# Optimization experiments

Measured on AMD Instinct MI355X. Metric: run time of the kernel, lower is better.

Reference implementation:

```python
import jax, jax.numpy as jnp
from jax import lax
import numpy as np


def _cum_masks(nd):
    # 4 nested cumulative masks over a 9-tap kernel: borders p=3,2,1,0
    ms = []
    for p in (3, 2, 1, 0):
        m = np.zeros((9,) * nd, np.float32)
        sl = tuple(slice(p, 9 - p) for _ in range(nd))
        m[sl] = 1.0
        ms.append(m)
    return jnp.asarray(np.stack(ms))  # (4, 9) or (4, 9, 9)


def _group_norm(x, w, b, groups, eps=1e-5):
    B, C, H, W = x.shape
    xg = x.reshape(B, groups, C // groups, H, W)
    mu = jnp.mean(xg, axis=(2, 3, 4), keepdims=True)
    var = jnp.var(xg, axis=(2, 3, 4), keepdims=True)
    xg = (xg - mu) * lax.rsqrt(var + eps)
    return xg.reshape(B, C, H, W) * w[None, :, None, None] + b[None, :, None, None]


def setup_inputs() -> dict:
    key = jax.random.key(0)
    ks = jax.random.split(key, 16)
    C = 256
    c = C // 4
    x = jax.random.normal(ks[0], (16, C, 128, 128), jnp.float32)
    W1 = jax.random.normal(ks[1], (1, 1, 9, 1, 1), jnp.float32)
    W2 = jax.random.normal(ks[2], (c, 1, 9, 9), jnp.float32)
    conv1_w = jax.random.normal(ks[3], (c, C, 1, 1), jnp.float32) * 0.05
    conv1_b = jax.random.normal(ks[4], (c,), jnp.float32) * 0.05
    conv2_w = jax.random.normal(ks[5], (C, c, 1, 1), jnp.float32) * 0.05
    conv2_b = jax.random.normal(ks[6], (C,), jnp.float32) * 0.05
    gn1_w = jnp.ones((c,), jnp.float32)
    gn1_b = jnp.zeros((c,), jnp.float32)
    gns_w = jnp.ones((c,), jnp.float32)
    gns_b = jnp.zeros((c,), jnp.float32)
    gn2_w = jnp.ones((C,), jnp.float32)
    gn2_b = jnp.zeros((C,), jnp.float32)
    return dict(x=x, W1=W1, W2=W2, conv1_w=conv1_w, conv1_b=conv1_b,
                conv2_w=conv2_w, conv2_b=conv2_b, gn1_w=gn1_w, gn1_b=gn1_b,
                gns_w=gns_w, gns_b=gns_b, gn2_w=gn2_w, gn2_b=gn2_b)


def reference(x, W1, W2, conv1_w, conv1_b, conv2_w, conv2_b,
              gn1_w, gn1_b, gns_w, gns_b, gn2_w, gn2_b):
    res = x
    # 1x1 conv + GN (bottleneck)
    h1 = jnp.einsum('bchw,oc->bohw', x, conv1_w[:, :, 0, 0]) + conv1_b[None, :, None, None]
    h1 = _group_norm(h1, gn1_w, gn1_b, 16)
    c = h1.shape[1]

    # --- branch A: multi-ring 1D conv along channel dim (conv3d, kernel (9,1,1)) ---
    m1 = _cum_masks(1)                                   # (4,9) cumulative masks
    r1 = m1 - jnp.concatenate([jnp.zeros_like(m1[:1]), m1[:-1]], 0)  # rings
    k1 = W1[0, 0, :, 0, 0]                               # (9,)
    a1 = jax.nn.softmax(jnp.sum(k1[None, :] * r1, 1) / (jnp.sum(r1, 1) + 1e-10))
    # linearity: softmax-weighted sum of 4 masked convs == one conv with weighted mask
    W1_eff = W1 * jnp.sum(a1[:, None] * m1, 0)[None, None, :, None, None]
    x3 = lax.conv_general_dilated(
        h1[:, None], W1_eff, (1, 1, 1), [(4, 4), (0, 0), (0, 0)],
        dimension_numbers=('NCDHW', 'OIDHW', 'NCDHW'))[:, 0]  # (b,c,h,w)

    # --- branch B: multi-ring 9x9 depthwise conv2d ---
    m2 = _cum_masks(2)                                   # (4,9,9)
    r2 = m2 - jnp.concatenate([jnp.zeros_like(m2[:1]), m2[:-1]], 0)
    num2 = jnp.sum(W2[None] * r2[:, None, None], axis=(1, 2, 3, 4))
    den2 = c * jnp.sum(r2, axis=(1, 2)) + 1e-10          # mask is (c,1,9,9) in torch
    a2 = jax.nn.softmax(num2 / den2)
    W2_eff = W2 * jnp.sum(a2[:, None, None] * m2, 0)[None, None]
    x_sa = lax.conv_general_dilated(
        h1, W2_eff, (1, 1), [(4, 4), (4, 4)],
        dimension_numbers=('NCHW', 'OIHW', 'NCHW'), feature_group_count=c)

    h = jax.nn.relu(_group_norm(x3 + x_sa, gns_w, gns_b, 16))
    out = jnp.einsum('bchw,oc->bohw', h, conv2_w[:, :, 0, 0]) + conv2_b[None, :, None, None]
    out = jax.nn.relu(_group_norm(out, gn2_w, gn2_b, 16))
    return out + res
```

## Files before the change

kernel.cpp:

```cpp
#include <hip/hip_runtime.h>
#include <math.h>

#define HW   16384
#define CC   256
#define cC   64
#define BB   16
#define CHW  (CC*HW)
#define cHW  (cC*HW)

#define WS_TB    0
#define WS_H1B   8388608
#define WS_RAWB  16777216
#define WS_W2E   50331648
#define WS_K1E   (WS_W2E + 5184)
#define WS_GN1A  (WS_K1E + 16)
#define WS_GNSA  (WS_GN1A + 512)
#define WS_GN2A  (WS_GNSA + 512)
#define WS_W1P   (WS_GN2A + 512)
#define WS_W2P   (WS_W1P + 8192)

typedef __attribute__((ext_vector_type(8))) short bf16x8;
typedef __attribute__((ext_vector_type(4))) float f32x4;

__device__ inline unsigned short f2bf(float f) {
    union { float f; unsigned u; } c; c.f = f;
    unsigned r = c.u + 0x7FFFu + ((c.u >> 16) & 1u);
    return (unsigned short)(r >> 16);
}
__device__ inline float bf2f(unsigned short h) {
    union { unsigned u; float f; } c; c.u = ((unsigned)h) << 16; return c.f;
}

__global__ void k_setup(const float* __restrict__ W1, const float* __restrict__ W2,
                        const float* __restrict__ c1w, const float* __restrict__ c2w,
                        float* __restrict__ k1e, float* __restrict__ w2e,
                        float* __restrict__ accz, unsigned short* __restrict__ w1p,
                        unsigned short* __restrict__ w2p) {
    __shared__ float tapsum[81];
    __shared__ float a2s[4];
    int tdx = threadIdx.x;
    for (int i = tdx; i < 1536; i += 128) accz[i] = 0.f;
    for (int e = tdx; e < 16384; e += 128) {
        int fi = e >> 9, rem = e & 511;
        int l = rem >> 3, j = rem & 7;
        int ks = fi >> 2, nf = fi & 3;
        int c = ks * 32 + (l >> 4) * 8 + j;
        int oc = nf * 16 + (l & 15);
        w1p[e] = f2bf(c1w[oc * 256 + c]);
    }
    for (int e = tdx; e < 16384; e += 128) {
        int fi = e >> 9, rem = e & 511;
        int l = rem >> 3, j = rem & 7;
        int ks = fi >> 4, nfg = fi & 15;
        int c = ks * 32 + (l >> 4) * 8 + j;
        int oc = nfg * 16 + (l & 15);
        w2p[e] = f2bf(c2w[oc * 64 + c]);
    }
    if (tdx < 81) {
        float s = 0.f;
        for (int ch = 0; ch < 64; ++ch) s += W2[ch * 81 + tdx];
        tapsum[tdx] = s;
    }
    __syncthreads();
    if (tdx == 0) {
        float ring[4] = {0.f, 0.f, 0.f, 0.f};
        for (int i = 0; i < 9; ++i)
            for (int j = 0; j < 9; ++j) {
                int d = max(abs(i - 4), abs(j - 4));
                int r = (d <= 1) ? 0 : (d - 1);
                ring[r] += tapsum[i * 9 + j];
            }
        float den2[4] = {576.f, 1024.f, 1536.f, 2048.f};
        float v[4], mx = -1e30f;
        for (int p = 0; p < 4; ++p) { v[p] = ring[p] / den2[p]; mx = fmaxf(mx, v[p]); }
        float se = 0.f;
        for (int p = 0; p < 4; ++p) { v[p] = expf(v[p] - mx); se += v[p]; }
        for (int p = 0; p < 4; ++p) a2s[p] = v[p] / se;
        float k1[9];
        for (int k = 0; k < 9; ++k) k1[k] = W1[k];
        float num[4];
        num[0] = k1[3] + k1[4] + k1[5];
        num[1] = k1[2] + k1[6];
        num[2] = k1[1] + k1[7];
        num[3] = k1[0] + k1[8];
        float den1[4] = {3.f, 2.f, 2.f, 2.f};
        mx = -1e30f;
        for (int p = 0; p < 4; ++p) { v[p] = num[p] / den1[p]; mx = fmaxf(mx, v[p]); }
        se = 0.f;
        for (int p = 0; p < 4; ++p) { v[p] = expf(v[p] - mx); se += v[p]; }
        float a1[4];
        for (int p = 0; p < 4; ++p) a1[p] = v[p] / se;
        float s1arr[5];
        s1arr[0] = 1.f; s1arr[1] = 1.f;
        s1arr[4] = a1[3]; s1arr[3] = a1[2] + a1[3]; s1arr[2] = a1[1] + s1arr[3];
        for (int k = 0; k < 9; ++k) { int d = abs(k - 4); k1e[k] = k1[k] * s1arr[d]; }
    }
    __syncthreads();
    float s2arr[5];
    s2arr[0] = 1.f; s2arr[1] = 1.f;
    s2arr[4] = a2s[3]; s2arr[3] = a2s[2] + a2s[3]; s2arr[2] = a2s[1] + s2arr[3];
    for (int idx = tdx; idx < 64 * 81; idx += 128) {
        int tap = idx % 81;
        int i = tap / 9, j = tap - i * 9;
        int d = max(abs(i - 4), abs(j - 4));
        w2e[idx] = W2[idx] * s2arr[d];
    }
}

__device__ inline void gn_affine(const float* __restrict__ acc, int b, int g,
                                 float inv_n, const float* __restrict__ gw,
                                 const float* __restrict__ gb, int ch,
                                 float& sc, float& sh) {
    float s = acc[(b * 16 + g) * 2], ss = acc[(b * 16 + g) * 2 + 1];
    float mu = s * inv_n;
    float var = ss * inv_n - mu * mu;
    float rstd = rsqrtf(var + 1e-5f);
    sc = gw[ch] * rstd;
    sh = gb[ch] - mu * sc;
}

__global__ __launch_bounds__(256) void k_conv1(const float* __restrict__ x,
        const unsigned short* __restrict__ w1p, const float* __restrict__ b1,
        unsigned short* __restrict__ h1, float* __restrict__ gn1a) {
    int bid = blockIdx.x;
    int b = bid >> 6, pt = bid & 63;
    int tid = threadIdx.x;
    int w = tid >> 6, lane = tid & 63;
    int l15 = lane & 15, lg = lane >> 4;
    int p_wave = pt * 256 + w * 64;
    const bf16x8* w1v = (const bf16x8*)w1p;
    f32x4 acc[4][4];
#pragma unroll
    for (int mf = 0; mf < 4; ++mf)
#pragma unroll
        for (int nf = 0; nf < 4; ++nf) acc[mf][nf] = (f32x4){0.f, 0.f, 0.f, 0.f};
    const float* xb = x + b * CHW;
#pragma unroll 1
    for (int ks = 0; ks < 8; ++ks) {
        int c0 = ks * 32 + lg * 8;
        bf16x8 afr[4];
#pragma unroll
        for (int mf = 0; mf < 4; ++mf) {
            const float* xp = xb + c0 * HW + p_wave + mf * 16 + l15;
            bf16x8 a;
#pragma unroll
            for (int j = 0; j < 8; ++j) a[j] = (short)f2bf(__builtin_nontemporal_load(xp + j * HW));
            afr[mf] = a;
        }
#pragma unroll
        for (int nf = 0; nf < 4; ++nf) {
            bf16x8 bfr = w1v[(ks * 4 + nf) * 64 + lane];
#pragma unroll
            for (int mf = 0; mf < 4; ++mf)
                acc[mf][nf] = __builtin_amdgcn_mfma_f32_16x16x32_bf16(afr[mf], bfr, acc[mf][nf], 0, 0, 0);
        }
    }
    __shared__ float red[4][16][2];
    unsigned short* hb = h1 + b * cHW;
#pragma unroll
    for (int nf = 0; nf < 4; ++nf) {
        int oc = nf * 16 + l15;
        float bias = b1[oc];
        float s = 0.f, ss = 0.f;
#pragma unroll
        for (int mf = 0; mf < 4; ++mf) {
            f32x4 v = acc[mf][nf];
            v[0] += bias; v[1] += bias; v[2] += bias; v[3] += bias;
            ushort4 hv = make_ushort4(f2bf(v[0]), f2bf(v[1]), f2bf(v[2]), f2bf(v[3]));
            *(ushort4*)(hb + oc * HW + p_wave + mf * 16 + lg * 4) = hv;
            s += v[0] + v[1] + v[2] + v[3];
            ss += v[0] * v[0] + v[1] * v[1] + v[2] * v[2] + v[3] * v[3];
        }
        s += __shfl_xor(s, 16, 64); ss += __shfl_xor(ss, 16, 64);
        s += __shfl_xor(s, 32, 64); ss += __shfl_xor(ss, 32, 64);
        s += __shfl_xor(s, 1, 64);  ss += __shfl_xor(ss, 1, 64);
        s += __shfl_xor(s, 2, 64);  ss += __shfl_xor(ss, 2, 64);
        if (lg == 0 && (l15 & 3) == 0) {
            int g = nf * 4 + (l15 >> 2);
            red[w][g][0] = s; red[w][g][1] = ss;
        }
    }
    __syncthreads();
    if (tid < 32) {
        int g = tid >> 1, c = tid & 1;
        float v = red[0][g][c] + red[1][g][c] + red[2][g][c] + red[3][g][c];
        atomicAdd(&gn1a[(b * 16 + g) * 2 + c], v);
    }
}

__global__ __launch_bounds__(256) void k_x3(const unsigned short* __restrict__ h1,
        const float* __restrict__ gn1a, const float* __restrict__ g1w,
        const float* __restrict__ g1b, const float* __restrict__ k1e,
        unsigned short* __restrict__ t) {
    int i = blockIdx.x * 256 + threadIdx.x;
    int b = i >> 13, p = (i & 8191) * 2;
    __shared__ float lsc[64], lsh[64], lke[9];
    if (threadIdx.x < 64) {
        int ch = threadIdx.x;
        float sc, sh;
        gn_affine(gn1a, b, ch >> 2, 1.f / 65536.f, g1w, g1b, ch, sc, sh);
        lsc[ch] = sc; lsh[ch] = sh;
    }
    if (threadIdx.x < 9) lke[threadIdx.x] = k1e[threadIdx.x];
    __syncthreads();
    const unsigned short* hb = h1 + b * cHW + p;
    float2 win[9];
#pragma unroll
    for (int k = 0; k < 9; ++k) {
        int ch = k - 4;
        if (ch >= 0) {
            ushort2 hv = *(const ushort2*)(hb + ch * HW);
            float s = lsc[ch], h = lsh[ch];
            win[k] = make_float2(fmaf(bf2f(hv.x), s, h), fmaf(bf2f(hv.y), s, h));
        } else win[k] = make_float2(0.f, 0.f);
    }
    unsigned short* tb = t + b * cHW + p;
#pragma unroll
    for (int ch = 0; ch < 64; ++ch) {
        float2 s = make_float2(0.f, 0.f);
#pragma unroll
        for (int k = 0; k < 9; ++k) {
            float kv = lke[k];
            s.x = fmaf(win[k].x, kv, s.x);
            s.y = fmaf(win[k].y, kv, s.y);
        }
        *(ushort2*)(tb + ch * HW) = make_ushort2(f2bf(s.x), f2bf(s.y));
#pragma unroll
        for (int k = 0; k < 8; ++k) win[k] = win[k + 1];
        int nc = ch + 5;
        if (nc < 64) {
            ushort2 hv = *(const ushort2*)(hb + nc * HW);
            float sN = lsc[nc], hN = lsh[nc];
            win[8] = make_float2(fmaf(bf2f(hv.x), sN, hN), fmaf(bf2f(hv.y), sN, hN));
        } else win[8] = make_float2(0.f, 0.f);
    }
}

__global__ __launch_bounds__(256) void k_xsa(const unsigned short* __restrict__ h1,
        const float* __restrict__ gn1a, const float* __restrict__ g1w,
        const float* __restrict__ g1b, const float* __restrict__ w2e,
        unsigned short* __restrict__ t, float* __restrict__ gnsa) {
    int bid = blockIdx.x;
    int b = bid >> 8, ch = (bid >> 2) & 63, rt = bid & 3;
    int r0 = rt * 32;
    int tid = threadIdx.x;
    float sc, sh;
    gn_affine(gn1a, b, ch >> 2, 1.f / 65536.f, g1w, g1b, ch, sc, sh);
    const unsigned short* hp = h1 + b * cHW + ch * HW;
    __shared__ float tile[40 * 136];
    for (int li = tid; li < 40 * 34; li += 256) {
        int row = li / 34, c4 = li - row * 34;
        int col = c4 * 4;
        int gr = r0 - 4 + row;
        float4 z = make_float4(0.f, 0.f, 0.f, 0.f);
        if (gr >= 0 && gr < 128 && c4 >= 1 && c4 <= 32) {
            int gc = col - 4;
            ushort4 hv = *(const ushort4*)(hp + gr * 128 + gc);
            z = make_float4(fmaf(bf2f(hv.x), sc, sh), fmaf(bf2f(hv.y), sc, sh),
                            fmaf(bf2f(hv.z), sc, sh), fmaf(bf2f(hv.w), sc, sh));
        }
        *(float4*)&tile[row * 136 + col] = z;
    }
    __syncthreads();
    int r4g = tid >> 5, c4g = tid & 31;
    int orow0 = r4g * 4, oc0 = c4g * 4;
    const float* wch = w2e + ch * 81;
    float acc[4][4];
#pragma unroll
    for (int r = 0; r < 4; ++r)
#pragma unroll
        for (int k = 0; k < 4; ++k) acc[r][k] = 0.f;
#pragma unroll
    for (int d = 0; d < 12; ++d) {
        const float* lr = &tile[(orow0 + d) * 136 + oc0];
        float v[12];
        *(float4*)&v[0] = *(const float4*)lr;
        *(float4*)&v[4] = *(const float4*)(lr + 4);
        *(float4*)&v[8] = *(const float4*)(lr + 8);
#pragma unroll
        for (int r = 0; r < 4; ++r) {
            if (r <= d && d - r <= 8) {
                const int i = d - r;
#pragma unroll
                for (int j = 0; j < 9; ++j) {
                    float wv = wch[i * 9 + j];
                    acc[r][0] = fmaf(v[j + 0], wv, acc[r][0]);
                    acc[r][1] = fmaf(v[j + 1], wv, acc[r][1]);
                    acc[r][2] = fmaf(v[j + 2], wv, acc[r][2]);
                    acc[r][3] = fmaf(v[j + 3], wv, acc[r][3]);
                }
            }
        }
    }
    float s = 0.f, ss = 0.f;
    unsigned short* tpb = t + b * cHW + ch * HW + (r0 + orow0) * 128 + oc0;
#pragma unroll
    for (int r = 0; r < 4; ++r) {
        unsigned short* tp = tpb + r * 128;
        ushort4 tv = *(const ushort4*)tp;
        float r0v = bf2f(tv.x) + acc[r][0];
        float r1v = bf2f(tv.y) + acc[r][1];
        float r2v = bf2f(tv.z) + acc[r][2];
        float r3v = bf2f(tv.w) + acc[r][3];
        *(ushort4*)tp = make_ushort4(f2bf(r0v), f2bf(r1v), f2bf(r2v), f2bf(r3v));
        s += r0v + r1v + r2v + r3v;
        ss += r0v * r0v + r1v * r1v + r2v * r2v + r3v * r3v;
    }
#pragma unroll
    for (int off = 32; off; off >>= 1) { s += __shfl_xor(s, off, 64); ss += __shfl_xor(ss, off, 64); }
    __shared__ float rs[4], rss[4];
    int lane = tid & 63, wv2 = tid >> 6;
    if (lane == 0) { rs[wv2] = s; rss[wv2] = ss; }
    __syncthreads();
    if (tid == 0) {
        int gi = (b * 16 + (ch >> 2)) * 2;
        atomicAdd(&gnsa[gi], rs[0] + rs[1] + rs[2] + rs[3]);
        atomicAdd(&gnsa[gi + 1], rss[0] + rss[1] + rss[2] + rss[3]);
    }
}

#define ROWU 68

__global__ __launch_bounds__(256) void k_conv2(const unsigned short* __restrict__ t,
        const float* __restrict__ gnsa, const float* __restrict__ gsw,
        const float* __restrict__ gsb, const unsigned short* __restrict__ w2p,
        const float* __restrict__ b2, unsigned short* __restrict__ raw,
        float* __restrict__ gn2a) {
    int bid = blockIdx.x;
    int b = bid >> 8, pt = bid & 255;
    int p0 = pt * 64;
    int tid = threadIdx.x;
    int w = tid >> 6, lane = tid & 63;
    int l15 = lane & 15, lg = lane >> 4;
    __shared__ float lsc[64], lsh[64];
    __shared__ unsigned short tps[64 * ROWU];
    __shared__ float red[4][4][2];
    if (tid < 64) {
        float sc, sh;
        gn_affine(gnsa, b, tid >> 2, 1.f / 65536.f, gsw, gsb, tid, sc, sh);
        lsc[tid] = sc; lsh[tid] = sh;
    }
    __syncthreads();
    {
        int ch = tid >> 2, c8 = tid & 3;
        float sc = lsc[ch], sh = lsh[ch];
        const unsigned short* tg = t + b * cHW + ch * HW + p0;
#pragma unroll
        for (int half = 0; half < 2; ++half) {
            int off = (c8 + half * 4) * 8;
            ushort4 a0 = *(const ushort4*)(tg + off);
            ushort4 a1 = *(const ushort4*)(tg + off + 4);
            ushort4 o0, o1;
            o0.x = f2bf(fmaxf(fmaf(bf2f(a0.x), sc, sh), 0.f));
            o0.y = f2bf(fmaxf(fmaf(bf2f(a0.y), sc, sh), 0.f));
            o0.z = f2bf(fmaxf(fmaf(bf2f(a0.z), sc, sh), 0.f));
            o0.w = f2bf(fmaxf(fmaf(bf2f(a0.w), sc, sh), 0.f));
            o1.x = f2bf(fmaxf(fmaf(bf2f(a1.x), sc, sh), 0.f));
            o1.y = f2bf(fmaxf(fmaf(bf2f(a1.y), sc, sh), 0.f));
            o1.z = f2bf(fmaxf(fmaf(bf2f(a1.z), sc, sh), 0.f));
            o1.w = f2bf(fmaxf(fmaf(bf2f(a1.w), sc, sh), 0.f));
            *(ushort4*)(&tps[ch * ROWU + off]) = o0;
            *(ushort4*)(&tps[ch * ROWU + off + 4]) = o1;
        }
    }
    __syncthreads();
    const bf16x8* w2v = (const bf16x8*)w2p;
    f32x4 acc[4][4];
#pragma unroll
    for (int mf = 0; mf < 4; ++mf)
#pragma unroll
        for (int nf = 0; nf < 4; ++nf) acc[mf][nf] = (f32x4){0.f, 0.f, 0.f, 0.f};
#pragma unroll
    for (int ks = 0; ks < 2; ++ks) {
        int kb = ks * 32 + lg * 8;
        bf16x8 afr[4];
#pragma unroll
        for (int mf = 0; mf < 4; ++mf) {
            int pos = mf * 16 + l15;
            bf16x8 a;
#pragma unroll
            for (int j = 0; j < 8; ++j) a[j] = (short)tps[(kb + j) * ROWU + pos];
            afr[mf] = a;
        }
#pragma unroll
        for (int nf = 0; nf < 4; ++nf) {
            int fi = ks * 16 + (w * 4 + nf);
            bf16x8 bfr = w2v[fi * 64 + lane];
#pragma unroll
            for (int mf = 0; mf < 4; ++mf)
                acc[mf][nf] = __builtin_amdgcn_mfma_f32_16x16x32_bf16(afr[mf], bfr, acc[mf][nf], 0, 0, 0);
        }
    }
    int oc0 = w * 64;
    unsigned short* ob = raw + b * CHW;
    float sred[4], ssred[4];
#pragma unroll
    for (int nf = 0; nf < 4; ++nf) {
        int oc = oc0 + nf * 16 + l15;
        float bias = b2[oc];
        float s = 0.f, ss = 0.f;
#pragma unroll
        for (int mf = 0; mf < 4; ++mf) {
            f32x4 v = acc[mf][nf];
            v[0] += bias; v[1] += bias; v[2] += bias; v[3] += bias;
            ushort4 hv = make_ushort4(f2bf(v[0]), f2bf(v[1]), f2bf(v[2]), f2bf(v[3]));
            *(ushort4*)(ob + oc * HW + p0 + mf * 16 + lg * 4) = hv;
            s += v[0] + v[1] + v[2] + v[3];
            ss += v[0] * v[0] + v[1] * v[1] + v[2] * v[2] + v[3] * v[3];
        }
#pragma unroll
        for (int off = 32; off; off >>= 1) { s += __shfl_xor(s, off, 64); ss += __shfl_xor(ss, off, 64); }
        sred[nf] = s; ssred[nf] = ss;
    }
    if (lane == 0) {
#pragma unroll
        for (int nf = 0; nf < 4; ++nf) { red[w][nf][0] = sred[nf]; red[w][nf][1] = ssred[nf]; }
    }
    __syncthreads();
    if (tid < 32) {
        int w_ = tid >> 3, nf = (tid >> 1) & 3, c = tid & 1;
        int g = w_ * 4 + nf;
        atomicAdd(&gn2a[(b * 16 + g) * 2 + c], red[w_][nf][c]);
    }
}

__global__ __launch_bounds__(256) void k_final(const float* __restrict__ x,
        const unsigned short* __restrict__ raw, const float* __restrict__ gn2a,
        const float* __restrict__ g2w, const float* __restrict__ g2b,
        float* __restrict__ out) {
    int tid = blockIdx.x * blockDim.x + threadIdx.x;
    const int total4 = (BB * CHW) / 4;
    int stride = gridDim.x * blockDim.x;
    for (int i = tid; i < total4; i += stride) {
        int e = i * 4;
        int b = e >> 22;
        int o = (e >> 14) & 255;
        float s, h;
        gn_affine(gn2a, b, o >> 4, 1.f / 262144.f, g2w, g2b, o, s, h);
        ushort4 rv = ((const ushort4*)raw)[i];
        f32x4 xv = __builtin_nontemporal_load((const f32x4*)x + i);
        f32x4 r;
        r[0] = fmaxf(fmaf(bf2f(rv.x), s, h), 0.f) + xv[0];
        r[1] = fmaxf(fmaf(bf2f(rv.y), s, h), 0.f) + xv[1];
        r[2] = fmaxf(fmaf(bf2f(rv.z), s, h), 0.f) + xv[2];
        r[3] = fmaxf(fmaf(bf2f(rv.w), s, h), 0.f) + xv[3];
        __builtin_nontemporal_store(r, (f32x4*)out + i);
    }
}

extern "C" void kernel_launch(void* const* d_in, const int* in_sizes, int n_in,
                              void* d_out, int out_size, void* d_ws, size_t ws_size,
                              hipStream_t stream) {
    (void)in_sizes; (void)n_in; (void)out_size; (void)ws_size;
    const float* x   = (const float*)d_in[0];
    const float* W1  = (const float*)d_in[1];
    const float* W2  = (const float*)d_in[2];
    const float* c1w = (const float*)d_in[3];
    const float* c1b = (const float*)d_in[4];
    const float* c2w = (const float*)d_in[5];
    const float* c2b = (const float*)d_in[6];
    const float* g1w = (const float*)d_in[7];
    const float* g1b = (const float*)d_in[8];
    const float* gsw = (const float*)d_in[9];
    const float* gsb = (const float*)d_in[10];
    const float* g2w = (const float*)d_in[11];
    const float* g2b = (const float*)d_in[12];
    float* out = (float*)d_out;
    float* ws  = (float*)d_ws;

    unsigned short* tb   = (unsigned short*)(ws + WS_TB);
    unsigned short* h1b  = (unsigned short*)(ws + WS_H1B);
    unsigned short* rawb = (unsigned short*)(ws + WS_RAWB);
    float* w2e  = ws + WS_W2E;
    float* k1e  = ws + WS_K1E;
    float* gn1a = ws + WS_GN1A;
    float* gnsa = ws + WS_GNSA;
    float* gn2a = ws + WS_GN2A;
    unsigned short* w1p = (unsigned short*)(ws + WS_W1P);
    unsigned short* w2p = (unsigned short*)(ws + WS_W2P);

    k_setup<<<1, 128, 0, stream>>>(W1, W2, c1w, c2w, k1e, w2e, gn1a, w1p, w2p);
    k_conv1<<<1024, 256, 0, stream>>>(x, w1p, c1b, h1b, gn1a);
    k_x3<<<512, 256, 0, stream>>>(h1b, gn1a, g1w, g1b, k1e, tb);
    k_xsa<<<4096, 256, 0, stream>>>(h1b, gn1a, g1w, g1b, w2e, tb, gnsa);
    k_conv2<<<4096, 256, 0, stream>>>(tb, gnsa, gsw, gsb, w2p, c2b, rawb, gn2a);
    k_final<<<4096, 256, 0, stream>>>(x, rawb, gn2a, g2w, g2b, out);
}
```

Baseline: 342.2 us.

## Recompute conv2 GEMM in final kernel instead of storing bf16 intermediate

The conv2 bottleneck GEMM is now run twice: once only to gather GroupNorm statistics, and again inside the final kernel, which applies GN2, ReLU and the residual add directly from the accumulators. This removes the write and re-read of the full-size bf16 intermediate buffer. In exchange it reads the small activation tensor twice and duplicates the MFMA work. Output stores also become tile-strided rather than one flat linear stream.

Measured after the change: 366.3 us. 7.0% more time.

```diff
diff --git a/kernel.cpp b/kernel.cpp
--- a/kernel.cpp
+++ b/kernel.cpp
@@ -10,7 +10,6 @@
 
 #define WS_TB    0
 #define WS_H1B   8388608
-#define WS_RAWB  16777216
 #define WS_W2E   50331648
 #define WS_K1E   (WS_W2E + 5184)
 #define WS_GN1A  (WS_K1E + 16)
@@ -321,20 +320,11 @@
 
 #define ROWU 68
 
-__global__ __launch_bounds__(256) void k_conv2(const unsigned short* __restrict__ t,
+__device__ inline void conv2_panel(const unsigned short* __restrict__ t,
         const float* __restrict__ gnsa, const float* __restrict__ gsw,
         const float* __restrict__ gsb, const unsigned short* __restrict__ w2p,
-        const float* __restrict__ b2, unsigned short* __restrict__ raw,
-        float* __restrict__ gn2a) {
-    int bid = blockIdx.x;
-    int b = bid >> 8, pt = bid & 255;
-    int p0 = pt * 64;
-    int tid = threadIdx.x;
-    int w = tid >> 6, lane = tid & 63;
-    int l15 = lane & 15, lg = lane >> 4;
-    __shared__ float lsc[64], lsh[64];
-    __shared__ unsigned short tps[64 * ROWU];
-    __shared__ float red[4][4][2];
+        int b, int p0, int tid, int w, int lane, int l15, int lg,
+        float* lsc, float* lsh, unsigned short* tps, f32x4 (&acc)[4][4]) {
     if (tid < 64) {
         float sc, sh;
         gn_affine(gnsa, b, tid >> 2, 1.f / 65536.f, gsw, gsb, tid, sc, sh);
@@ -365,7 +355,6 @@
     }
     __syncthreads();
     const bf16x8* w2v = (const bf16x8*)w2p;
-    f32x4 acc[4][4];
 #pragma unroll
     for (int mf = 0; mf < 4; ++mf)
 #pragma unroll
@@ -391,20 +380,33 @@
                 acc[mf][nf] = __builtin_amdgcn_mfma_f32_16x16x32_bf16(afr[mf], bfr, acc[mf][nf], 0, 0, 0);
         }
     }
-    int oc0 = w * 64;
-    unsigned short* ob = raw + b * CHW;
+}
+
+__global__ __launch_bounds__(256) void k_conv2s(const unsigned short* __restrict__ t,
+        const float* __restrict__ gnsa, const float* __restrict__ gsw,
+        const float* __restrict__ gsb, const unsigned short* __restrict__ w2p,
+        const float* __restrict__ b2, float* __restrict__ gn2a) {
+    int bid = blockIdx.x;
+    int b = bid >> 8, pt = bid & 255;
+    int p0 = pt * 64;
+    int tid = threadIdx.x;
+    int w = tid >> 6, lane = tid & 63;
+    int l15 = lane & 15, lg = lane >> 4;
+    __shared__ float lsc[64], lsh[64];
+    __shared__ unsigned short tps[64 * ROWU];
+    __shared__ float red[4][4][2];
+    f32x4 acc[4][4];
+    conv2_panel(t, gnsa, gsw, gsb, w2p, b, p0, tid, w, lane, l15, lg, lsc, lsh, tps, acc);
     float sred[4], ssred[4];
 #pragma unroll
     for (int nf = 0; nf < 4; ++nf) {
-        int oc = oc0 + nf * 16 + l15;
+        int oc = w * 64 + nf * 16 + l15;
         float bias = b2[oc];
         float s = 0.f, ss = 0.f;
 #pragma unroll
         for (int mf = 0; mf < 4; ++mf) {
             f32x4 v = acc[mf][nf];
             v[0] += bias; v[1] += bias; v[2] += bias; v[3] += bias;
-            ushort4 hv = make_ushort4(f2bf(v[0]), f2bf(v[1]), f2bf(v[2]), f2bf(v[3]));
-            *(ushort4*)(ob + oc * HW + p0 + mf * 16 + lg * 4) = hv;
             s += v[0] + v[1] + v[2] + v[3];
             ss += v[0] * v[0] + v[1] * v[1] + v[2] * v[2] + v[3] * v[3];
         }
@@ -424,27 +426,42 @@
     }
 }
 
-__global__ __launch_bounds__(256) void k_final(const float* __restrict__ x,
-        const unsigned short* __restrict__ raw, const float* __restrict__ gn2a,
+__global__ __launch_bounds__(256) void k_final(const unsigned short* __restrict__ t,
+        const float* __restrict__ gnsa, const float* __restrict__ gsw,
+        const float* __restrict__ gsb, const unsigned short* __restrict__ w2p,
+        const float* __restrict__ b2, const float* __restrict__ gn2a,
         const float* __restrict__ g2w, const float* __restrict__ g2b,
-        float* __restrict__ out) {
-    int tid = blockIdx.x * blockDim.x + threadIdx.x;
-    const int total4 = (BB * CHW) / 4;
-    int stride = gridDim.x * blockDim.x;
-    for (int i = tid; i < total4; i += stride) {
-        int e = i * 4;
-        int b = e >> 22;
-        int o = (e >> 14) & 255;
-        float s, h;
-        gn_affine(gn2a, b, o >> 4, 1.f / 262144.f, g2w, g2b, o, s, h);
-        ushort4 rv = ((const ushort4*)raw)[i];
-        f32x4 xv = __builtin_nontemporal_load((const f32x4*)x + i);
-        f32x4 r;
-        r[0] = fmaxf(fmaf(bf2f(rv.x), s, h), 0.f) + xv[0];
-        r[1] = fmaxf(fmaf(bf2f(rv.y), s, h), 0.f) + xv[1];
-        r[2] = fmaxf(fmaf(bf2f(rv.z), s, h), 0.f) + xv[2];
-        r[3] = fmaxf(fmaf(bf2f(rv.w), s, h), 0.f) + xv[3];
-        __builtin_nontemporal_store(r, (f32x4*)out + i);
+        const float* __restrict__ x, float* __restrict__ out) {
+    int bid = blockIdx.x;
+    int b = bid >> 8, pt = bid & 255;
+    int p0 = pt * 64;
+    int tid = threadIdx.x;
+    int w = tid >> 6, lane = tid & 63;
+    int l15 = lane & 15, lg = lane >> 4;
+    __shared__ float lsc[64], lsh[64];
+    __shared__ unsigned short tps[64 * ROWU];
+    f32x4 acc[4][4];
+    conv2_panel(t, gnsa, gsw, gsb, w2p, b, p0, tid, w, lane, l15, lg, lsc, lsh, tps, acc);
+    const float* xb = x + b * CHW;
+    float* ob = out + b * CHW;
+#pragma unroll
+    for (int nf = 0; nf < 4; ++nf) {
+        int oc = w * 64 + nf * 16 + l15;
+        float bias = b2[oc];
+        float s2, h2;
+        gn_affine(gn2a, b, oc >> 4, 1.f / 262144.f, g2w, g2b, oc, s2, h2);
+#pragma unroll
+        for (int mf = 0; mf < 4; ++mf) {
+            int off = oc * HW + p0 + mf * 16 + lg * 4;
+            f32x4 xv = __builtin_nontemporal_load((const f32x4*)(xb + off));
+            f32x4 v = acc[mf][nf];
+            f32x4 r;
+            r[0] = fmaxf(fmaf(v[0] + bias, s2, h2), 0.f) + xv[0];
+            r[1] = fmaxf(fmaf(v[1] + bias, s2, h2), 0.f) + xv[1];
+            r[2] = fmaxf(fmaf(v[2] + bias, s2, h2), 0.f) + xv[2];
+            r[3] = fmaxf(fmaf(v[3] + bias, s2, h2), 0.f) + xv[3];
+            __builtin_nontemporal_store(r, (f32x4*)(ob + off));
+        }
     }
 }
 
@@ -470,7 +487,6 @@
 
     unsigned short* tb   = (unsigned short*)(ws + WS_TB);
     unsigned short* h1b  = (unsigned short*)(ws + WS_H1B);
-    unsigned short* rawb = (unsigned short*)(ws + WS_RAWB);
     float* w2e  = ws + WS_W2E;
     float* k1e  = ws + WS_K1E;
     float* gn1a = ws + WS_GN1A;
@@ -483,6 +499,6 @@
     k_conv1<<<1024, 256, 0, stream>>>(x, w1p, c1b, h1b, gn1a);
     k_x3<<<512, 256, 0, stream>>>(h1b, gn1a, g1w, g1b, k1e, tb);
     k_xsa<<<4096, 256, 0, stream>>>(h1b, gn1a, g1w, g1b, w2e, tb, gnsa);
-    k_conv2<<<4096, 256, 0, stream>>>(tb, gnsa, gsw, gsb, w2p, c2b, rawb, gn2a);
-    k_final<<<4096, 256, 0, stream>>>(x, rawb, gn2a, g2w, g2b, out);
-}
+    k_conv2s<<<4096, 256, 0, stream>>>(tb, gnsa, gsw, gsb, w2p, c2b, gn2a);
+    k_final<<<4096, 256, 0, stream>>>(tb, gnsa, gsw, gsb, w2p, c2b, gn2a, g2w, g2b, x, out);
+}
```
